# Performance work log

Measured on AMD Instinct MI355X. Metric: run time of the kernel, lower is better.

The kernel has to match this reference:

```python
import jax, jax.numpy as jnp
import numpy as np

B, L, D, H, PD = 1, 512, 1024, 16, 128
HW = D // H  # 64


def _layernorm(x, g, b, eps=1e-5):
    mu = jnp.mean(x, axis=-1, keepdims=True)
    var = jnp.var(x, axis=-1, keepdims=True)
    return (x - mu) * jax.lax.rsqrt(var + eps) * g + b


def setup_inputs() -> dict:
    key = jax.random.key(0)
    ks = jax.random.split(key, 16)
    s = 0.02
    return {
        "sequence_state": jax.random.normal(ks[0], (B, L, D), jnp.float32),
        "pairwise_state": jax.random.normal(ks[1], (B, L, L, PD), jnp.float32),
        "mask": jnp.ones((B, L), dtype=bool),
        # layernorm before attention
        "ln1_g": jnp.ones((D,), jnp.float32),
        "ln1_b": jnp.zeros((D,), jnp.float32),
        # attention params (weights stored [in, out])
        "proj_w": jax.random.normal(ks[2], (D, 3 * H * HW), jnp.float32) * s,
        "g_w": jax.random.normal(ks[3], (D, H * HW), jnp.float32) * s,
        "g_b": jnp.ones((H * HW,), jnp.float32),
        "o_w": jax.random.normal(ks[4], (H * HW, D), jnp.float32) * s,
        "o_b": jnp.zeros((D,), jnp.float32),
        # pair-to-sequence bias
        "p2s_ln_g": jnp.ones((PD,), jnp.float32),
        "p2s_ln_b": jnp.zeros((PD,), jnp.float32),
        "p2s_w": jax.random.normal(ks[5], (PD, H), jnp.float32) * s,
        # residue MLP
        "mlp_ln_g": jnp.ones((D,), jnp.float32),
        "mlp_ln_b": jnp.zeros((D,), jnp.float32),
        "mlp_w1": jax.random.normal(ks[6], (D, 4 * D), jnp.float32) * s,
        "mlp_b1": jnp.zeros((4 * D,), jnp.float32),
        "mlp_w2": jax.random.normal(ks[7], (4 * D, D), jnp.float32) * s,
        "mlp_b2": jnp.zeros((D,), jnp.float32),
    }


def reference(sequence_state, pairwise_state, mask,
              ln1_g, ln1_b, proj_w, g_w, g_b, o_w, o_b,
              p2s_ln_g, p2s_ln_b, p2s_w,
              mlp_ln_g, mlp_ln_b, mlp_w1, mlp_b1, mlp_w2, mlp_b2):
    # PairToSequence: LN over pairwise feature dim, then project to per-head bias
    z = _layernorm(pairwise_state, p2s_ln_g, p2s_ln_b)
    bias = jnp.einsum("bqkp,ph->bhqk", z, p2s_w)  # [B,H,L,L]

    # Pre-attention layernorm
    y = _layernorm(sequence_state, ln1_g, ln1_b)

    # Gated attention with pairwise bias
    t = (y @ proj_w).reshape(B, L, H, 3 * HW)
    q, k, v = jnp.split(t, 3, axis=-1)  # each [B,L,H,HW]
    q = q * (HW ** -0.5)
    a = jnp.einsum("bqhc,bkhc->bhqk", q, k) + bias
    a = jnp.where(mask[:, None, None, :], a, -jnp.inf)
    a = jax.nn.softmax(a, axis=-1)
    o = jnp.einsum("bhqk,bkhc->bqhc", a, v).reshape(B, L, H * HW)
    gate = jax.nn.sigmoid(y @ g_w + g_b)
    o = (gate * o) @ o_w + o_b

    # residual (dropout=0 -> identity)
    s = sequence_state + o

    # ResidueMLP: x + Linear(ReLU(Linear(LN(x))))
    h = _layernorm(s, mlp_ln_g, mlp_ln_b)
    h = jax.nn.relu(h @ mlp_w1 + mlp_b1) @ mlp_w2 + mlp_b2
    return s + h
```

## Files before the change

### kernel.cpp

```cpp
#include <hip/hip_runtime.h>


typedef __attribute__((ext_vector_type(8))) short bfrag;
typedef __attribute__((ext_vector_type(4))) float f32x4;
typedef unsigned short ushort_t;
typedef unsigned int u32;

#define AS1 __attribute__((address_space(1)))
#define AS3 __attribute__((address_space(3)))

__device__ __forceinline__ void gll16(const void* g, void* l) {
  __builtin_amdgcn_global_load_lds((const AS1 u32*)g, (AS3 u32*)l, 16, 0, 0);
}

__device__ __forceinline__ unsigned short f2b(float x) {
  union { float f; unsigned u; } a; a.f = x;
  unsigned r = a.u + 0x7fffu + ((a.u >> 16) & 1u);
  return (unsigned short)(r >> 16);
}
__device__ __forceinline__ unsigned pack2(float a, float b) {
  return (unsigned)f2b(a) | ((unsigned)f2b(b) << 16);
}
__device__ __forceinline__ float b2f(ushort_t u) {
  union { float f; unsigned v; } a; a.v = ((unsigned)u) << 16; return a.f;
}

#define OFF_BIASH ((size_t)0)
#define OFF_Y     ((size_t)8388608)
#define OFF_QS    (OFF_Y    + (size_t)1048576)
#define OFF_KS    (OFF_QS   + (size_t)1048576)
#define OFF_VT    (OFF_KS   + (size_t)1048576)
#define OFF_GATE  (OFF_VT   + (size_t)1048576)
#define OFF_OG    (OFF_GATE + (size_t)2097152)
#define OFF_S     (OFF_OG   + (size_t)1048576)
#define OFF_HLN   (OFF_S    + (size_t)2097152)
#define OFF_H1    (OFF_HLN  + (size_t)1048576)
#define OFF_WPG   (OFF_H1   + (size_t)4194304)
#define OFF_WO    (OFF_WPG  + (size_t)8388608)
#define OFF_W1    (OFF_WO   + (size_t)2097152)
#define OFF_W2    (OFF_W1   + (size_t)8388608)

__device__ __forceinline__ void transp_tile(
    const float* __restrict__ W, ushort_t* __restrict__ Wt, int K, int N,
    int bx, int by, int tid, float* smem) {
  float (*tile)[65] = (float(*)[65])smem;
  int n0 = bx * 64, k0 = by * 64;
  int tr = tid >> 4, tc = (tid & 15) * 4;
#pragma unroll
  for (int i = 0; i < 4; i++) {
    int r = tr + i * 16;
    f32x4 v = __builtin_nontemporal_load(
        (const f32x4*)&W[(long)(k0 + r) * N + n0 + tc]);
    tile[r][tc] = v.x; tile[r][tc + 1] = v.y; tile[r][tc + 2] = v.z; tile[r][tc + 3] = v.w;
  }
  __syncthreads();
  int nr = tid >> 2, kk = (tid & 3) * 16;
  ushort_t* dst = Wt + (long)(n0 + nr) * K + k0 + kk;
  uint4 q;
  q.x = pack2(tile[kk + 0][nr], tile[kk + 1][nr]);
  q.y = pack2(tile[kk + 2][nr], tile[kk + 3][nr]);
  q.z = pack2(tile[kk + 4][nr], tile[kk + 5][nr]);
  q.w = pack2(tile[kk + 6][nr], tile[kk + 7][nr]);
  *(uint4*)dst = q;
  uint4 q2;
  q2.x = pack2(tile[kk + 8][nr],  tile[kk + 9][nr]);
  q2.y = pack2(tile[kk + 10][nr], tile[kk + 11][nr]);
  q2.z = pack2(tile[kk + 12][nr], tile[kk + 13][nr]);
  q2.w = pack2(tile[kk + 14][nr], tile[kk + 15][nr]);
  *(uint4*)(dst + 8) = q2;
}

__global__ __launch_bounds__(256) void mega1(
    const float* __restrict__ pw,
    const float* __restrict__ p2s_g, const float* __restrict__ p2s_b,
    const float* __restrict__ p2s_w,
    const float* __restrict__ proj_w, const float* __restrict__ g_w,
    const float* __restrict__ o_w, const float* __restrict__ w1,
    const float* __restrict__ w2,
    const float* __restrict__ seq, const float* __restrict__ ln1_g,
    const float* __restrict__ ln1_b, const float* __restrict__ o_b,
    ushort_t* __restrict__ biasH, ushort_t* __restrict__ wpg,
    ushort_t* __restrict__ wo, ushort_t* __restrict__ w1t,
    ushort_t* __restrict__ w2t, ushort_t* __restrict__ ybf,
    float* __restrict__ sbuf) {
  __shared__ float smemF[5920];
  const int id = blockIdx.x, t = threadIdx.x;

  if (id < 4096) {
    ushort_t* wb  = (ushort_t*)smemF;
    ushort_t* zsb = wb + 2048;
    ushort_t* res = zsb + 64 * 136;
    const int w = t >> 6, lane = t & 63, ln = lane & 15, quad = lane >> 4;
    const long pair0 = (long)id * 64;
    const int p = w * 16 + (lane >> 2);
    const int j = lane & 3;

#pragma unroll
    for (int i = t; i < 2048; i += 256) {
      int f = i >> 4, hh = i & 15;
      int chunk = f >> 5, q2 = (f >> 3) & 3, jj = f & 7;
      wb[(chunk * 64 + q2 * 16 + hh) * 8 + jj] = f2b(p2s_w[i]);
    }

    const float* xbase = pw + (pair0 + p) * 128 + j * 4;
    f32x4 xv[8];
#pragma unroll
    for (int q = 0; q < 8; q++)
      xv[q] = __builtin_nontemporal_load((const f32x4*)(xbase + q * 16));
    float s = 0.f, sq = 0.f;
#pragma unroll
    for (int q = 0; q < 8; q++) {
      s  += xv[q].x + xv[q].y + xv[q].z + xv[q].w;
      sq += xv[q].x*xv[q].x + xv[q].y*xv[q].y + xv[q].z*xv[q].z + xv[q].w*xv[q].w;
    }
    s += __shfl_xor(s, 1); s += __shfl_xor(s, 2);
    sq += __shfl_xor(sq, 1); sq += __shfl_xor(sq, 2);
    float mu = s * (1.f / 128.f);
    float rs = rsqrtf(sq * (1.f / 128.f) - mu * mu + 1e-5f);

#pragma unroll
    for (int q = 0; q < 8; q++) {
      f32x4 gv = *(const f32x4*)(p2s_g + j * 4 + q * 16);
      f32x4 bv = *(const f32x4*)(p2s_b + j * 4 + q * 16);
      uint2 o;
      o.x = pack2((xv[q].x - mu) * rs * gv.x + bv.x, (xv[q].y - mu) * rs * gv.y + bv.y);
      o.y = pack2((xv[q].z - mu) * rs * gv.z + bv.z, (xv[q].w - mu) * rs * gv.w + bv.w);
      *(uint2*)&zsb[p * 136 + q * 16 + j * 4] = o;
    }
    __syncthreads();

    f32x4 acc = (f32x4){0.f, 0.f, 0.f, 0.f};
#pragma unroll
    for (int chunk = 0; chunk < 4; chunk++) {
      bfrag a  = *(const bfrag*)&zsb[(w * 16 + ln) * 136 + chunk * 32 + quad * 8];
      bfrag bf = *(const bfrag*)&wb[(chunk * 64 + quad * 16 + ln) * 8];
      acc = __builtin_amdgcn_mfma_f32_16x16x32_bf16(a, bf, acc, 0, 0, 0);
    }
    *(uint2*)&res[ln * 68 + w * 16 + quad * 4] =
        (uint2){pack2(acc[0], acc[1]), pack2(acc[2], acc[3])};
    __syncthreads();
    {
      int hh = t >> 4, base = (t & 15) * 4;
      *(uint2*)&biasH[(long)hh * 262144 + pair0 + base] =
          *(const uint2*)&res[hh * 68 + base];
    }
  } else if (id < 7424) {
    int j = id - 4096;
    if (j < 768)       transp_tile(proj_w, wpg, 1024, 3072, j % 48, j / 48, t, smemF);
    else if (j < 1024) { j -= 768;  transp_tile(g_w, wpg + (long)3072 * 1024, 1024, 1024, j % 16, j / 16, t, smemF); }
    else if (j < 1280) { j -= 1024; transp_tile(o_w, wo, 1024, 1024, j % 16, j / 16, t, smemF); }
    else if (j < 2304) { j -= 1280; transp_tile(w1, w1t, 1024, 4096, j % 64, j / 64, t, smemF); }
    else               { j -= 2304; transp_tile(w2, w2t, 4096, 1024, j % 16, j / 16, t, smemF); }
  } else {
    int row = id - 7424;
    long base = (long)row * 1024 + t * 4;
    float4 v = *(const float4*)(seq + base);
    float4 ob = *(const float4*)(o_b + t * 4);
    float4 sv; sv.x = v.x + ob.x; sv.y = v.y + ob.y; sv.z = v.z + ob.z; sv.w = v.w + ob.w;
    *(float4*)(sbuf + base) = sv;
    float s  = v.x + v.y + v.z + v.w;
    float sq = v.x*v.x + v.y*v.y + v.z*v.z + v.w*v.w;
#pragma unroll
    for (int k = 1; k < 64; k <<= 1) { s += __shfl_xor(s, k); sq += __shfl_xor(sq, k); }
    if ((t & 63) == 0) { smemF[t >> 6] = s; smemF[4 + (t >> 6)] = sq; }
    __syncthreads();
    s  = smemF[0] + smemF[1] + smemF[2] + smemF[3];
    sq = smemF[4] + smemF[5] + smemF[6] + smemF[7];
    float mu = s * (1.f / 1024.f);
    float rsd = rsqrtf(sq * (1.f / 1024.f) - mu * mu + 1e-5f);
    float4 gv = *(const float4*)(ln1_g + t * 4);
    float4 bv = *(const float4*)(ln1_b + t * 4);
    uint2 o;
    o.x = pack2((v.x - mu) * rsd * gv.x + bv.x, (v.y - mu) * rsd * gv.y + bv.y);
    o.y = pack2((v.z - mu) * rsd * gv.z + bv.z, (v.w - mu) * rsd * gv.w + bv.w);
    *(uint2*)(ybf + base) = o;
  }
}

template <int EPI>
__global__ __launch_bounds__(256) void gemm64(
    const ushort_t* __restrict__ A, const ushort_t* __restrict__ Bt,
    int lda, int ldb, int Ksplit,
    const float* __restrict__ bias1,
    float* __restrict__ outF, ushort_t* __restrict__ outH, int ldc,
    ushort_t* __restrict__ qs, ushort_t* __restrict__ ks,
    ushort_t* __restrict__ vt, float* __restrict__ gatebuf) {
  __shared__ ushort_t As[4][64 * 32];
  __shared__ ushort_t Bs[4][64 * 32];
  const int tid = threadIdx.x;
  const int w = tid >> 6, lane = tid & 63;
  const int ln = lane & 15, quad = lane >> 4;
  const int wm = w >> 1, wn = w & 1;
  const int m0 = blockIdx.y * 64, n0 = blockIdx.x * 64;
  const int z = blockIdx.z;
  const int Koff = (EPI == 7) ? z * Ksplit : 0;

  const ushort_t* ga = A  + (long)(m0 + (tid >> 2)) * lda + Koff + (tid & 3) * 8;
  const ushort_t* gb = Bt + (long)(n0 + (tid >> 2)) * ldb + Koff + (tid & 3) * 8;
  unsigned wofs = __builtin_amdgcn_readfirstlane(w * 1024);
  char* lAw = (char*)&As[0][0] + wofs;
  char* lBw = (char*)&Bs[0][0] + wofs;

  f32x4 acc[2][2];
#pragma unroll
  for (int i = 0; i < 2; i++)
#pragma unroll
    for (int jj = 0; jj < 2; jj++) acc[i][jj] = (f32x4){0.f, 0.f, 0.f, 0.f};

  auto stage = [&](int t) {
    int boff = (t & 3) * 4096;
    gll16(ga + t * 32, lAw + boff);
    gll16(gb + t * 32, lBw + boff);
  };
  auto body = [&](int b) {
    const ushort_t* Ab = (const ushort_t*)((const char*)&As[0][0] + b * 4096);
    const ushort_t* Bb = (const ushort_t*)((const char*)&Bs[0][0] + b * 4096);
    bfrag a0 = *(const bfrag*)&Ab[(wm * 32 + ln) * 32 + quad * 8];
    bfrag a1 = *(const bfrag*)&Ab[(wm * 32 + 16 + ln) * 32 + quad * 8];
    bfrag b0 = *(const bfrag*)&Bb[(wn * 32 + ln) * 32 + quad * 8];
    bfrag b1 = *(const bfrag*)&Bb[(wn * 32 + 16 + ln) * 32 + quad * 8];
    acc[0][0] = __builtin_amdgcn_mfma_f32_16x16x32_bf16(a0, b0, acc[0][0], 0, 0, 0);
    acc[0][1] = __builtin_amdgcn_mfma_f32_16x16x32_bf16(a0, b1, acc[0][1], 0, 0, 0);
    acc[1][0] = __builtin_amdgcn_mfma_f32_16x16x32_bf16(a1, b0, acc[1][0], 0, 0, 0);
    acc[1][1] = __builtin_amdgcn_mfma_f32_16x16x32_bf16(a1, b1, acc[1][1], 0, 0, 0);
  };

  const int niter = Ksplit >> 5;
  stage(0);
  if (niter > 1) stage(1);
  if (niter > 2) stage(2);

  int k = 0;
  for (; k + 2 < niter; ++k) {
    asm volatile("s_waitcnt vmcnt(4)" ::: "memory");
    __builtin_amdgcn_s_barrier();
    __builtin_amdgcn_sched_barrier(0);
    if (k + 3 < niter) stage(k + 3);
    body(k & 3);
  }
  for (; k < niter; ++k) {
    if (k + 1 < niter) { asm volatile("s_waitcnt vmcnt(2)" ::: "memory"); }
    else               { asm volatile("s_waitcnt vmcnt(0)" ::: "memory"); }
    __builtin_amdgcn_s_barrier();
    __builtin_amdgcn_sched_barrier(0);
    body(k & 3);
  }

#pragma unroll
  for (int am = 0; am < 2; am++) {
#pragma unroll
    for (int bn = 0; bn < 2; bn++) {
      int ocol = n0 + wn * 32 + bn * 16 + ln;
#pragma unroll
      for (int r = 0; r < 4; r++) {
        int orow = m0 + wm * 32 + am * 16 + quad * 4 + r;
        float v = acc[am][bn][r];
        if (EPI == 3) {
          v = fmaxf(v + bias1[ocol], 0.f);
          outH[(long)orow * ldc + ocol] = f2b(v);
        } else if (EPI == 6) {
          if (ocol < 3072) {
            int h = ocol / 192, jq = ocol - h * 192;
            if (jq < 64)       qs[((long)h * 512 + orow) * 64 + jq] = f2b(v * 0.125f);
            else if (jq < 128) ks[((long)h * 512 + orow) * 64 + (jq - 64)] = f2b(v);
            else               vt[((long)h * 64 + (jq - 128)) * 512 + orow] = f2b(v);
          } else {
            int gcol = ocol - 3072;
            float gv = v + bias1[gcol];
            gatebuf[(long)orow * 1024 + gcol] = 1.f / (1.f + __expf(-gv));
          }
        } else {
          atomicAdd(&outF[(long)orow * ldc + ocol], v);
        }
      }
    }
  }
}

__global__ __launch_bounds__(256) void flash_attn(
    const ushort_t* __restrict__ qs, const ushort_t* __restrict__ ks,
    const ushort_t* __restrict__ vt, const ushort_t* __restrict__ biasH,
    const float* __restrict__ gate, ushort_t* __restrict__ og) {
  __shared__ ushort_t Qs[32 * 72];
  __shared__ ushort_t Ks[64 * 72];
  __shared__ ushort_t Vs[64 * 72];
  __shared__ ushort_t Ps[4][16 * 40];
  const int tid = threadIdx.x;
  const int w = tid >> 6, lane = tid & 63, ln = lane & 15, quad = lane >> 4;
  const int wm = w >> 1, wn = w & 1;
  const int h = blockIdx.x, q0 = blockIdx.y * 32;

  { int r = tid >> 3, c = (tid & 7) * 8;
    *(uint4*)&Qs[r * 72 + c] = *(const uint4*)(qs + ((long)(h * 512 + q0 + r)) * 64 + c); }

  float m_[4], l_[4];
  f32x4 Oacc[4];
#pragma unroll
  for (int i = 0; i < 4; i++) { m_[i] = -1e30f; l_[i] = 0.f; Oacc[i] = (f32x4){0.f,0.f,0.f,0.f}; }

  const int rkv = tid >> 2, ckv = (tid & 3) * 16;

  for (int kt = 0; kt < 8; kt++) {
    const int k0 = kt * 64;
    __syncthreads();
    { const ushort_t* sk = ks + ((long)(h * 512 + k0 + rkv)) * 64 + ckv;
      *(uint4*)&Ks[rkv * 72 + ckv]     = *(const uint4*)sk;
      *(uint4*)&Ks[rkv * 72 + ckv + 8] = *(const uint4*)(sk + 8);
      const ushort_t* sv = vt + ((long)(h * 64 + rkv)) * 512 + k0 + ckv;
      *(uint4*)&Vs[rkv * 72 + ckv]     = *(const uint4*)sv;
      *(uint4*)&Vs[rkv * 72 + ckv + 8] = *(const uint4*)(sv + 8); }

    f32x4 acc[2];
    const ushort_t* bp = biasH + ((long)(h * 512 + q0 + wm * 16 + quad * 4)) * 512
                         + k0 + wn * 32 + ln;
#pragma unroll
    for (int t4 = 0; t4 < 2; t4++)
#pragma unroll
      for (int rr = 0; rr < 4; rr++)
        acc[t4][rr] = b2f(bp[(long)rr * 512 + t4 * 16]);

    __syncthreads();
#pragma unroll
    for (int s = 0; s < 2; s++) {
      bfrag a = *(const bfrag*)&Qs[(wm * 16 + ln) * 72 + s * 32 + quad * 8];
#pragma unroll
      for (int t4 = 0; t4 < 2; t4++) {
        bfrag b = *(const bfrag*)&Ks[(wn * 32 + t4 * 16 + ln) * 72 + s * 32 + quad * 8];
        acc[t4] = __builtin_amdgcn_mfma_f32_16x16x32_bf16(a, b, acc[t4], 0, 0, 0);
      }
    }

    float mt[4];
#pragma unroll
    for (int rr = 0; rr < 4; rr++) mt[rr] = fmaxf(acc[0][rr], acc[1][rr]);
#pragma unroll
    for (int xm = 1; xm < 16; xm <<= 1)
#pragma unroll
      for (int rr = 0; rr < 4; rr++) mt[rr] = fmaxf(mt[rr], __shfl_xor(mt[rr], xm));
    float al[4];
#pragma unroll
    for (int rr = 0; rr < 4; rr++) {
      float mn = fmaxf(m_[rr], mt[rr]);
      al[rr] = __expf(m_[rr] - mn);
      m_[rr] = mn;
    }
#pragma unroll
    for (int t4 = 0; t4 < 2; t4++)
#pragma unroll
      for (int rr = 0; rr < 4; rr++)
        acc[t4][rr] = __expf(acc[t4][rr] - m_[rr]);
    float rsl[4];
#pragma unroll
    for (int rr = 0; rr < 4; rr++) rsl[rr] = acc[0][rr] + acc[1][rr];
#pragma unroll
    for (int xm = 1; xm < 16; xm <<= 1)
#pragma unroll
      for (int rr = 0; rr < 4; rr++) rsl[rr] += __shfl_xor(rsl[rr], xm);
#pragma unroll
    for (int rr = 0; rr < 4; rr++) l_[rr] = l_[rr] * al[rr] + rsl[rr];
#pragma unroll
    for (int t4 = 0; t4 < 4; t4++)
#pragma unroll
      for (int rr = 0; rr < 4; rr++) Oacc[t4][rr] *= al[rr];

#pragma unroll
    for (int t4 = 0; t4 < 2; t4++)
#pragma unroll
      for (int rr = 0; rr < 4; rr++)
        Ps[w][(quad * 4 + rr) * 40 + t4 * 16 + ln] = f2b(acc[t4][rr]);
    __builtin_amdgcn_wave_barrier();
    __builtin_amdgcn_s_waitcnt(0xC07F);
    __builtin_amdgcn_wave_barrier();

    {
      bfrag a = *(const bfrag*)&Ps[w][ln * 40 + quad * 8];
#pragma unroll
      for (int t4 = 0; t4 < 4; t4++) {
        bfrag b = *(const bfrag*)&Vs[(t4 * 16 + ln) * 72 + wn * 32 + quad * 8];
        Oacc[t4] = __builtin_amdgcn_mfma_f32_16x16x32_bf16(a, b, Oacc[t4], 0, 0, 0);
      }
    }
  }

  __syncthreads();
  float* ml = (float*)(void*)Ks;
  if (ln == 0)
#pragma unroll
    for (int rr = 0; rr < 4; rr++) {
      ml[(w * 16 + quad * 4 + rr) * 2 + 0] = m_[rr];
      ml[(w * 16 + quad * 4 + rr) * 2 + 1] = l_[rr];
    }
  __syncthreads();
  const int pw_ = wm * 2 + (wn ^ 1);
  float a_self[4];
#pragma unroll
  for (int rr = 0; rr < 4; rr++) {
    float mo = ml[(pw_ * 16 + quad * 4 + rr) * 2 + 0];
    float lo = ml[(pw_ * 16 + quad * 4 + rr) * 2 + 1];
    float mF = fmaxf(m_[rr], mo);
    a_self[rr] = __expf(m_[rr] - mF);
    l_[rr] = l_[rr] * a_self[rr] + lo * __expf(mo - mF);
  }
  float* Of = (float*)(void*)Vs;
  if (wn == 1) {
#pragma unroll
    for (int t4 = 0; t4 < 4; t4++)
#pragma unroll
      for (int rr = 0; rr < 4; rr++)
        Of[(wm * 16 + quad * 4 + rr) * 68 + t4 * 16 + ln] = Oacc[t4][rr] * a_self[rr];
  }
  __syncthreads();
  if (wn == 0) {
#pragma unroll
    for (int t4 = 0; t4 < 4; t4++) {
#pragma unroll
      for (int rr = 0; rr < 4; rr++) {
        int grow = q0 + wm * 16 + quad * 4 + rr;
        int gcol = h * 64 + t4 * 16 + ln;
        float v = Oacc[t4][rr] * a_self[rr]
                + Of[(wm * 16 + quad * 4 + rr) * 68 + t4 * 16 + ln];
        v /= l_[rr];
        og[(long)grow * 1024 + gcol] = f2b(v * gate[(long)grow * 1024 + gcol]);
      }
    }
  }
}

__global__ __launch_bounds__(256) void ln2(
    const float* __restrict__ sbuf, const float* __restrict__ g,
    const float* __restrict__ b, const float* __restrict__ b2,
    ushort_t* __restrict__ hln, float* __restrict__ out) {
  __shared__ float ps[8];
  int row = blockIdx.x, t = threadIdx.x;
  long base = (long)row * 1024 + t * 4;
  float4 v = *(const float4*)(sbuf + base);
  float4 b2v = *(const float4*)(b2 + t * 4);
  float4 ov; ov.x = v.x + b2v.x; ov.y = v.y + b2v.y; ov.z = v.z + b2v.z; ov.w = v.w + b2v.w;
  *(float4*)(out + base) = ov;
  float s  = v.x + v.y + v.z + v.w;
  float sq = v.x*v.x + v.y*v.y + v.z*v.z + v.w*v.w;
#pragma unroll
  for (int k = 1; k < 64; k <<= 1) { s += __shfl_xor(s, k); sq += __shfl_xor(sq, k); }
  if ((t & 63) == 0) { ps[t >> 6] = s; ps[4 + (t >> 6)] = sq; }
  __syncthreads();
  s  = ps[0] + ps[1] + ps[2] + ps[3];
  sq = ps[4] + ps[5] + ps[6] + ps[7];
  float mu = s * (1.f / 1024.f);
  float rsd = rsqrtf(sq * (1.f / 1024.f) - mu * mu + 1e-5f);
  float4 gv = *(const float4*)(g + t * 4);
  float4 bv = *(const float4*)(b + t * 4);
  uint2 o;
  o.x = pack2((v.x - mu) * rsd * gv.x + bv.x, (v.y - mu) * rsd * gv.y + bv.y);
  o.y = pack2((v.z - mu) * rsd * gv.z + bv.z, (v.w - mu) * rsd * gv.w + bv.w);
  *(uint2*)(hln + base) = o;
}

extern "C" void kernel_launch(void* const* d_in, const int* in_sizes, int n_in,
                              void* d_out, int out_size, void* d_ws, size_t ws_size,
                              hipStream_t stream) {
  const float* seq    = (const float*)d_in[0];
  const float* pw     = (const float*)d_in[1];
  const float* ln1_g  = (const float*)d_in[3];
  const float* ln1_b  = (const float*)d_in[4];
  const float* proj_w = (const float*)d_in[5];
  const float* g_w    = (const float*)d_in[6];
  const float* g_b    = (const float*)d_in[7];
  const float* o_w    = (const float*)d_in[8];
  const float* o_b    = (const float*)d_in[9];
  const float* p2s_g  = (const float*)d_in[10];
  const float* p2s_b  = (const float*)d_in[11];
  const float* p2s_w  = (const float*)d_in[12];
  const float* mlp_g  = (const float*)d_in[13];
  const float* mlp_bb = (const float*)d_in[14];
  const float* w1     = (const float*)d_in[15];
  const float* b1     = (const float*)d_in[16];
  const float* w2     = (const float*)d_in[17];
  const float* b2     = (const float*)d_in[18];
  float* out = (float*)d_out;
  char* ws = (char*)d_ws;

  ushort_t* biasH = (ushort_t*)(ws + OFF_BIASH);
  ushort_t* ybf   = (ushort_t*)(ws + OFF_Y);
  ushort_t* qs    = (ushort_t*)(ws + OFF_QS);
  ushort_t* ks    = (ushort_t*)(ws + OFF_KS);
  ushort_t* vt    = (ushort_t*)(ws + OFF_VT);
  float* gatebuf  = (float*)(ws + OFF_GATE);
  ushort_t* og    = (ushort_t*)(ws + OFF_OG);
  float* sbuf     = (float*)(ws + OFF_S);
  ushort_t* hln   = (ushort_t*)(ws + OFF_HLN);
  ushort_t* h1    = (ushort_t*)(ws + OFF_H1);
  ushort_t* wpg   = (ushort_t*)(ws + OFF_WPG);
  ushort_t* wo    = (ushort_t*)(ws + OFF_WO);
  ushort_t* w1t   = (ushort_t*)(ws + OFF_W1);
  ushort_t* w2t   = (ushort_t*)(ws + OFF_W2);

  mega1<<<7936, 256, 0, stream>>>(pw, p2s_g, p2s_b, p2s_w,
                                  proj_w, g_w, o_w, w1, w2,
                                  seq, ln1_g, ln1_b, o_b,
                                  biasH, wpg, wo, w1t, w2t, ybf, sbuf);
  gemm64<6><<<dim3(64, 8, 1), 256, 0, stream>>>(ybf, wpg, 1024, 1024, 1024,
                                                g_b, nullptr, nullptr, 0,
                                                qs, ks, vt, gatebuf);
  flash_attn<<<dim3(16, 16), 256, 0, stream>>>(qs, ks, vt, biasH, gatebuf, og);
  gemm64<7><<<dim3(16, 8, 4), 256, 0, stream>>>(og, wo, 1024, 1024, 256,
                                                nullptr, sbuf, nullptr, 1024,
                                                nullptr, nullptr, nullptr, nullptr);
  ln2<<<512, 256, 0, stream>>>(sbuf, mlp_g, mlp_bb, b2, hln, out);
  gemm64<3><<<dim3(64, 8, 1), 256, 0, stream>>>(hln, w1t, 1024, 1024, 1024,
                                                b1, nullptr, h1, 4096,
                                                nullptr, nullptr, nullptr, nullptr);
  gemm64<7><<<dim3(16, 8, 4), 256, 0, stream>>>(h1, w2t, 4096, 4096, 1024,
                                                nullptr, out, nullptr, 1024,
                                                nullptr, nullptr, nullptr, nullptr);
}
```

Baseline: 332.8 us.

## Prefetch K/V/bias tiles into registers in attention and use split-K partial buffers

The flash attention loop now prefetches the next K, V and bias tile into registers while the current tile is computed, and stages the bias tile in shared memory instead of scattered global reads. The output-projection split-K GEMM writes four partial buffers instead of issuing atomics, and ln2 sums them together with the residual and o_b, which removes the sbuf initialization from mega1. The atomic split-K GEMM also rotates its column blocks by z so the slices spread their atomic traffic. Costs are more registers in attention, extra workspace, and extra partial-buffer reads in ln2.

```diff
diff --git a/kernel.cpp b/kernel.cpp
--- a/kernel.cpp
+++ b/kernel.cpp
@@ -39,6 +39,7 @@
 #define OFF_WO    (OFF_WPG  + (size_t)8388608)
 #define OFF_W1    (OFF_WO   + (size_t)2097152)
 #define OFF_W2    (OFF_W1   + (size_t)8388608)
+#define OFF_PART  (OFF_W2   + (size_t)8388608)
 
 __device__ __forceinline__ void transp_tile(
     const float* __restrict__ W, ushort_t* __restrict__ Wt, int K, int N,
@@ -78,11 +79,10 @@
     const float* __restrict__ o_w, const float* __restrict__ w1,
     const float* __restrict__ w2,
     const float* __restrict__ seq, const float* __restrict__ ln1_g,
-    const float* __restrict__ ln1_b, const float* __restrict__ o_b,
+    const float* __restrict__ ln1_b,
     ushort_t* __restrict__ biasH, ushort_t* __restrict__ wpg,
     ushort_t* __restrict__ wo, ushort_t* __restrict__ w1t,
-    ushort_t* __restrict__ w2t, ushort_t* __restrict__ ybf,
-    float* __restrict__ sbuf) {
+    ushort_t* __restrict__ w2t, ushort_t* __restrict__ ybf) {
   __shared__ float smemF[5920];
   const int id = blockIdx.x, t = threadIdx.x;
 
@@ -155,9 +155,6 @@
     int row = id - 7424;
     long base = (long)row * 1024 + t * 4;
     float4 v = *(const float4*)(seq + base);
-    float4 ob = *(const float4*)(o_b + t * 4);
-    float4 sv; sv.x = v.x + ob.x; sv.y = v.y + ob.y; sv.z = v.z + ob.z; sv.w = v.w + ob.w;
-    *(float4*)(sbuf + base) = sv;
     float s  = v.x + v.y + v.z + v.w;
     float sq = v.x*v.x + v.y*v.y + v.z*v.z + v.w*v.w;
 #pragma unroll
@@ -191,9 +188,10 @@
   const int w = tid >> 6, lane = tid & 63;
   const int ln = lane & 15, quad = lane >> 4;
   const int wm = w >> 1, wn = w & 1;
-  const int m0 = blockIdx.y * 64, n0 = blockIdx.x * 64;
   const int z = blockIdx.z;
-  const int Koff = (EPI == 7) ? z * Ksplit : 0;
+  const int nblk = (EPI == 7) ? ((blockIdx.x + z * 4) & 15) : blockIdx.x;
+  const int m0 = blockIdx.y * 64, n0 = nblk * 64;
+  const int Koff = (EPI >= 7) ? z * Ksplit : 0;
 
   const ushort_t* ga = A  + (long)(m0 + (tid >> 2)) * lda + Koff + (tid & 3) * 8;
   const ushort_t* gb = Bt + (long)(n0 + (tid >> 2)) * ldb + Koff + (tid & 3) * 8;
@@ -269,8 +267,10 @@
             float gv = v + bias1[gcol];
             gatebuf[(long)orow * 1024 + gcol] = 1.f / (1.f + __expf(-gv));
           }
+        } else if (EPI == 7) {
+          atomicAdd(&outF[(long)orow * ldc + ocol], v);
         } else {
-          atomicAdd(&outF[(long)orow * ldc + ocol], v);
+          outF[((long)z << 19) + (long)orow * 1024 + ocol] = v;
         }
       }
     }
@@ -284,6 +284,7 @@
   __shared__ ushort_t Qs[32 * 72];
   __shared__ ushort_t Ks[64 * 72];
   __shared__ ushort_t Vs[64 * 72];
+  __shared__ ushort_t Bb[32 * 72];
   __shared__ ushort_t Ps[4][16 * 40];
   const int tid = threadIdx.x;
   const int w = tid >> 6, lane = tid & 63, ln = lane & 15, quad = lane >> 4;
@@ -299,27 +300,43 @@
   for (int i = 0; i < 4; i++) { m_[i] = -1e30f; l_[i] = 0.f; Oacc[i] = (f32x4){0.f,0.f,0.f,0.f}; }
 
   const int rkv = tid >> 2, ckv = (tid & 3) * 16;
-
-  for (int kt = 0; kt < 8; kt++) {
+  const int rb = tid >> 3,  cb = (tid & 7) * 8;
+
+  uint4 kA0, kA1, vA0, vA1, bA, kB0, kB1, vB0, vB1, bB;
+
+  auto ldr = [&](int kt, uint4& K0, uint4& K1, uint4& V0, uint4& V1, uint4& BB) {
     const int k0 = kt * 64;
-    __syncthreads();
-    { const ushort_t* sk = ks + ((long)(h * 512 + k0 + rkv)) * 64 + ckv;
-      *(uint4*)&Ks[rkv * 72 + ckv]     = *(const uint4*)sk;
-      *(uint4*)&Ks[rkv * 72 + ckv + 8] = *(const uint4*)(sk + 8);
-      const ushort_t* sv = vt + ((long)(h * 64 + rkv)) * 512 + k0 + ckv;
-      *(uint4*)&Vs[rkv * 72 + ckv]     = *(const uint4*)sv;
-      *(uint4*)&Vs[rkv * 72 + ckv + 8] = *(const uint4*)(sv + 8); }
+    const ushort_t* sk = ks + ((long)(h * 512 + k0 + rkv)) * 64 + ckv;
+    K0 = *(const uint4*)sk;
+    K1 = *(const uint4*)(sk + 8);
+    const ushort_t* sv = vt + ((long)(h * 64 + rkv)) * 512 + k0 + ckv;
+    V0 = *(const uint4*)sv;
+    V1 = *(const uint4*)(sv + 8);
+    BB = *(const uint4*)(biasH + ((long)(h * 512 + q0 + rb)) * 512 + k0 + cb);
+  };
+
+  auto tile = [&](int kt, uint4& K0, uint4& K1, uint4& V0, uint4& V1, uint4& BB,
+                  uint4& nK0, uint4& nK1, uint4& nV0, uint4& nV1, uint4& nBB) {
+    asm volatile("s_waitcnt lgkmcnt(0)" ::: "memory");
+    __builtin_amdgcn_s_barrier();
+    __builtin_amdgcn_sched_barrier(0);
+    *(uint4*)&Ks[rkv * 72 + ckv]     = K0;
+    *(uint4*)&Ks[rkv * 72 + ckv + 8] = K1;
+    *(uint4*)&Vs[rkv * 72 + ckv]     = V0;
+    *(uint4*)&Vs[rkv * 72 + ckv + 8] = V1;
+    *(uint4*)&Bb[rb * 72 + cb]       = BB;
+    if (kt < 7) ldr(kt + 1, nK0, nK1, nV0, nV1, nBB);
+    asm volatile("s_waitcnt lgkmcnt(0)" ::: "memory");
+    __builtin_amdgcn_s_barrier();
+    __builtin_amdgcn_sched_barrier(0);
 
     f32x4 acc[2];
-    const ushort_t* bp = biasH + ((long)(h * 512 + q0 + wm * 16 + quad * 4)) * 512
-                         + k0 + wn * 32 + ln;
 #pragma unroll
     for (int t4 = 0; t4 < 2; t4++)
 #pragma unroll
       for (int rr = 0; rr < 4; rr++)
-        acc[t4][rr] = b2f(bp[(long)rr * 512 + t4 * 16]);
-
-    __syncthreads();
+        acc[t4][rr] = b2f(Bb[(wm * 16 + quad * 4 + rr) * 72 + wn * 32 + t4 * 16 + ln]);
+
 #pragma unroll
     for (int s = 0; s < 2; s++) {
       bfrag a = *(const bfrag*)&Qs[(wm * 16 + ln) * 72 + s * 32 + quad * 8];
@@ -380,6 +397,13 @@
         Oacc[t4] = __builtin_amdgcn_mfma_f32_16x16x32_bf16(a, b, Oacc[t4], 0, 0, 0);
       }
     }
+  };
+
+  ldr(0, kA0, kA1, vA0, vA1, bA);
+#pragma unroll
+  for (int kt2 = 0; kt2 < 8; kt2 += 2) {
+    tile(kt2,     kA0, kA1, vA0, vA1, bA, kB0, kB1, vB0, vB1, bB);
+    tile(kt2 + 1, kB0, kB1, vB0, vB1, bB, kA0, kA1, vA0, vA1, bA);
   }
 
   __syncthreads();
@@ -427,13 +451,21 @@
 }
 
 __global__ __launch_bounds__(256) void ln2(
-    const float* __restrict__ sbuf, const float* __restrict__ g,
+    const float* __restrict__ seq, const float* __restrict__ part,
+    const float* __restrict__ o_b, const float* __restrict__ g,
     const float* __restrict__ b, const float* __restrict__ b2,
     ushort_t* __restrict__ hln, float* __restrict__ out) {
   __shared__ float ps[8];
   int row = blockIdx.x, t = threadIdx.x;
   long base = (long)row * 1024 + t * 4;
-  float4 v = *(const float4*)(sbuf + base);
+  float4 v = *(const float4*)(seq + base);
+  float4 ob = *(const float4*)(o_b + t * 4);
+  v.x += ob.x; v.y += ob.y; v.z += ob.z; v.w += ob.w;
+#pragma unroll
+  for (int z = 0; z < 4; z++) {
+    float4 pv = *(const float4*)(part + ((long)z << 19) + base);
+    v.x += pv.x; v.y += pv.y; v.z += pv.z; v.w += pv.w;
+  }
   float4 b2v = *(const float4*)(b2 + t * 4);
   float4 ov; ov.x = v.x + b2v.x; ov.y = v.y + b2v.y; ov.z = v.z + b2v.z; ov.w = v.w + b2v.w;
   *(float4*)(out + base) = ov;
@@ -486,26 +518,26 @@
   ushort_t* vt    = (ushort_t*)(ws + OFF_VT);
   float* gatebuf  = (float*)(ws + OFF_GATE);
   ushort_t* og    = (ushort_t*)(ws + OFF_OG);
-  float* sbuf     = (float*)(ws + OFF_S);
   ushort_t* hln   = (ushort_t*)(ws + OFF_HLN);
   ushort_t* h1    = (ushort_t*)(ws + OFF_H1);
   ushort_t* wpg   = (ushort_t*)(ws + OFF_WPG);
   ushort_t* wo    = (ushort_t*)(ws + OFF_WO);
   ushort_t* w1t   = (ushort_t*)(ws + OFF_W1);
   ushort_t* w2t   = (ushort_t*)(ws + OFF_W2);
+  float* part4    = (float*)(ws + OFF_PART);
 
   mega1<<<7936, 256, 0, stream>>>(pw, p2s_g, p2s_b, p2s_w,
                                   proj_w, g_w, o_w, w1, w2,
-                                  seq, ln1_g, ln1_b, o_b,
-                                  biasH, wpg, wo, w1t, w2t, ybf, sbuf);
+                                  seq, ln1_g, ln1_b,
+                                  biasH, wpg, wo, w1t, w2t, ybf);
   gemm64<6><<<dim3(64, 8, 1), 256, 0, stream>>>(ybf, wpg, 1024, 1024, 1024,
                                                 g_b, nullptr, nullptr, 0,
                                                 qs, ks, vt, gatebuf);
   flash_attn<<<dim3(16, 16), 256, 0, stream>>>(qs, ks, vt, biasH, gatebuf, og);
-  gemm64<7><<<dim3(16, 8, 4), 256, 0, stream>>>(og, wo, 1024, 1024, 256,
-                                                nullptr, sbuf, nullptr, 1024,
+  gemm64<8><<<dim3(16, 8, 4), 256, 0, stream>>>(og, wo, 1024, 1024, 256,
+                                                nullptr, part4, nullptr, 1024,
                                                 nullptr, nullptr, nullptr, nullptr);
-  ln2<<<512, 256, 0, stream>>>(sbuf, mlp_g, mlp_bb, b2, hln, out);
+  ln2<<<512, 256, 0, stream>>>(seq, part4, o_b, mlp_g, mlp_bb, b2, hln, out);
   gemm64<3><<<dim3(64, 8, 1), 256, 0, stream>>>(hln, w1t, 1024, 1024, 1024,
                                                 b1, nullptr, h1, 4096,
                                                 nullptr, nullptr, nullptr, nullptr);
```

Result: no change. 328.6 us (-1.3%).
